# Kernel optimization log

Measured on AMD Instinct MI355X. Metric: run time of the kernel, lower is better.

The kernel has to match this reference:

```python
import jax, jax.numpy as jnp
import numpy as np
from jax import lax

EPS = 1e-8


def setup_inputs() -> dict:
    key = jax.random.key(0)
    k1, k2, k3, k4, k5 = jax.random.split(key, 5)
    b, c_in, c_out, h, w_sp, k, z = 8, 256, 256, 128, 128, 3, 512
    return {
        "x": jax.random.normal(k1, (b, c_in, h, w_sp), dtype=jnp.float32),
        "w": jax.random.normal(k2, (b, z), dtype=jnp.float32),
        "weight": jax.random.normal(k3, (c_out, c_in, k, k), dtype=jnp.float32),
        "affine_w": jax.random.normal(k4, (c_in, z), dtype=jnp.float32) * 0.02,
        "affine_b": jax.random.normal(k5, (c_in,), dtype=jnp.float32) * 0.02,
    }


def reference(x, w, weight, affine_w, affine_b):
    # style: [b, c_in] -> broadcast over (out_ch, kh, kw); +1 as in StyleGAN2
    style = w @ affine_w.T + affine_b + 1.0                      # [b, c_in]
    wgt = weight[None] * style[:, None, :, None, None]           # [b, O, I, kh, kw]
    # demodulation
    denom = lax.rsqrt(jnp.sum(wgt * wgt, axis=(2, 3, 4)) + EPS)  # [b, O]
    wgt = wgt * denom[:, :, None, None, None]

    # per-sample conv (equivalent to groups=b grouped conv), 'same' padding
    def conv_one(xi, wi):
        # xi: [I, H, W], wi: [O, I, kh, kw]
        return lax.conv_general_dilated(
            xi[None], wi, window_strides=(1, 1), padding="SAME",
            dimension_numbers=("NCHW", "OIHW", "NCHW"))[0]

    return jax.vmap(conv_one)(x, wgt)                            # [b, O, H, W]
```

## Files before the change

kernel.cpp:

```cpp
#include <hip/hip_runtime.h>

#define EPS 1e-8f

using short8 = __attribute__((ext_vector_type(8))) short;
using f32x16 = __attribute__((ext_vector_type(16))) float;
typedef unsigned short u16;

#define WAITV(N) asm volatile("s_waitcnt vmcnt(" #N ")" ::: "memory")
#define BARRIER() do { __builtin_amdgcn_s_barrier(); \
                       asm volatile("" ::: "memory"); } while (0)

__device__ __forceinline__ u16 f2bf(float f) {
    union { float f; unsigned u; } v; v.f = f;
    unsigned u = v.u;
    return (u16)((u + 0x7FFFu + ((u >> 16) & 1u)) >> 16);
}

__device__ __forceinline__ void g2l16(const void* gsrc, void* ldst) {
    __builtin_amdgcn_global_load_lds(
        (const __attribute__((address_space(1))) unsigned int*)gsrc,
        (__attribute__((address_space(3))) unsigned int*)ldst, 16, 0, 0);
}

__global__ void style_kernel(const float* __restrict__ w,
                             const float* __restrict__ affine_w,
                             const float* __restrict__ affine_b,
                             float* __restrict__ style) {
    int b = blockIdx.x;
    int i = threadIdx.x;
    __shared__ float wb[512];
    for (int z = threadIdx.x; z < 512; z += 256) wb[z] = w[b * 512 + z];
    __syncthreads();
    const float* aw = affine_w + i * 512;
    float acc = 0.f;
#pragma unroll 4
    for (int z = 0; z < 512; z += 4) {
        float4 a4 = *reinterpret_cast<const float4*>(aw + z);
        acc += a4.x * wb[z] + a4.y * wb[z + 1] + a4.z * wb[z + 2] + a4.w * wb[z + 3];
    }
    style[b * 256 + i] = acc + affine_b[i] + 1.0f;
}

__global__ void modw_kernel(const float* __restrict__ weight,
                            const float* __restrict__ style,
                            u16* __restrict__ wgt) {
    int b = blockIdx.x >> 8;
    int o = blockIdx.x & 255;
    int ic = threadIdx.x;
    float s = style[b * 256 + ic];
    const float* wp = weight + (size_t)(o * 256 + ic) * 9;
    float m[9];
    float ss = 0.f;
#pragma unroll
    for (int t = 0; t < 9; ++t) { m[t] = wp[t] * s; ss += m[t] * m[t]; }
#pragma unroll
    for (int off = 32; off > 0; off >>= 1) ss += __shfl_down(ss, off);
    __shared__ float part[4];
    int lane = threadIdx.x & 63, wid = threadIdx.x >> 6;
    if (lane == 0) part[wid] = ss;
    __syncthreads();
    float denom = rsqrtf(part[0] + part[1] + part[2] + part[3] + EPS);
    int g = ic >> 3, j = ic & 7;
#pragma unroll
    for (int t = 0; t < 9; ++t) {
        size_t idx = ((((size_t)(b * 9 + t) * 32 + g) * 256 + o) << 3) + j;
        wgt[idx] = f2bf(m[t] * denom);
    }
}

__global__ __launch_bounds__(256) void xform_kernel(const float* __restrict__ x,
                                                    u16* __restrict__ xb) {
    int s = blockIdx.x * 256 + threadIdx.x;
    int w = s & 127, h = (s >> 7) & 127, g = (s >> 14) & 31, b = s >> 19;
    const float* xp = x + (((size_t)(b * 256 + g * 8) * 128 + h) * 128 + w);
    union { u16 u[8]; short8 v; } pk;
#pragma unroll
    for (int j = 0; j < 8; ++j) pk.u[j] = f2bf(xp[(size_t)j * 16384]);
    *reinterpret_cast<short8*>(&xb[(size_t)s * 8]) = pk.v;
}

__global__ __launch_bounds__(256, 2) void conv_kernel(
    const u16* __restrict__ xb,
    const u16* __restrict__ wgt,
    float* __restrict__ out) {

    __shared__ __align__(16) u16 Xs[4][4][130][8];
    __shared__ __align__(16) u16 As[5][4][128][8];
    __shared__ __align__(16) u16 trash[1024];

    int bid = blockIdx.x;
    int swz = (bid & 7) * 128 + (bid >> 3);
    int ht = swz & 63, ot = (swz >> 6) & 1, b = swz >> 7;
    int h0 = ht * 2;

    int tid = threadIdx.x, lane = tid & 63, wid = tid >> 6;
    int wm = wid >> 1, wr = wid & 1;
    int l31 = lane & 31, lh = lane >> 5;

    auto stageA = [&](int cc, int tt, int ring) {
        const u16* wbase = wgt + ((size_t)(b * 9 + tt) * 32) * 2048;
#pragma unroll
        for (int k = 0; k < 2; ++k) {
            int seg = wid * 2 + k, g = seg >> 1, oh = seg & 1;
            const u16* src = wbase +
                ((size_t)(cc * 4 + g) * 256 + ot * 128 + oh * 64 + lane) * 8;
            g2l16(src, &As[ring][g][oh * 64][0]);
        }
    };

    {
        short8 z = {0, 0, 0, 0, 0, 0, 0, 0};
        short8* p0 = reinterpret_cast<short8*>(&Xs[0][0][0][0]);
        for (int i = tid; i < 2080; i += 256) p0[i] = z;
    }
    __syncthreads();

    stageA(0, 0, 0); stageA(0, 1, 1); stageA(0, 2, 2);
    {
        int hr = h0 + wid - 1;
        bool oob = ((unsigned)hr >= 128u);
        int hc = oob ? 0 : hr;
#pragma unroll
        for (int k = 0; k < 8; ++k) {
            int g = k >> 1, half = k & 1;
            const u16* src = xb +
                ((((size_t)(b * 32 + g)) * 128 + hc) * 128 + half * 64 + lane) * 8;
            void* dst = oob ? (void*)trash : (void*)&Xs[wid][g][1 + half * 64][0];
            g2l16(src, dst);
        }
    }
    WAITV(0);
    BARRIER();

    f32x16 acc[2][4] = {};
    short8 xr[8];
    int rr = 0, rw = 3, cs = 0, ts = 3;

    auto doPhase = [&](int t, int ring) {
        int kh = t / 3, kw = t - kh * 3;
        short8 af[2][2], bx8[2][4];
#pragma unroll
        for (int kk = 0; kk < 2; ++kk)
#pragma unroll
            for (int mi = 0; mi < 2; ++mi)
                af[kk][mi] = *reinterpret_cast<const short8*>(
                    &As[ring][kk * 2 + lh][wm * 64 + mi * 32 + l31][0]);
#pragma unroll
        for (int kk = 0; kk < 2; ++kk)
#pragma unroll
            for (int ni = 0; ni < 4; ++ni)
                bx8[kk][ni] = *reinterpret_cast<const short8*>(
                    &Xs[wr + kh][kk * 2 + lh][ni * 32 + l31 + kw][0]);
        __builtin_amdgcn_s_setprio(1);
#pragma unroll
        for (int mi = 0; mi < 2; ++mi)
#pragma unroll
            for (int ni = 0; ni < 4; ++ni)
#pragma unroll
                for (int kk = 0; kk < 2; ++kk)
                    acc[mi][ni] = __builtin_amdgcn_mfma_f32_32x32x16_bf16(
                        af[kk][mi], bx8[kk][ni], acc[mi][ni], 0, 0, 0);
        __builtin_amdgcn_s_setprio(0);
    };

    int hr = h0 + wid - 1;
    bool hValid = ((unsigned)hr < 128u);
    int hc = hValid ? hr : 0;

    for (int c = 0; c < 7; ++c) {
#pragma unroll
        for (int t = 0; t < 9; ++t) {
            stageA(cs, ts, rw);
            if (++ts == 9) { ts = 0; ++cs; }
            if (t == 5) {
#pragma unroll
                for (int k = 0; k < 8; ++k) {
                    int g = k >> 1, half = k & 1;
                    xr[k] = *reinterpret_cast<const short8*>(xb +
                        ((((size_t)(b * 32 + (c + 1) * 4 + g)) * 128 + hc) * 128 +
                         half * 64 + lane) * 8);
                }
            }
            doPhase(t, rr);
            rr = (rr == 4) ? 0 : rr + 1;
            rw = (rw == 4) ? 0 : rw + 1;
            if (t == 1 || t == 3) { WAITV(2);  BARRIER(); }
            else if (t == 5)      { WAITV(10); BARRIER(); }
            else if (t == 7)      { WAITV(12); BARRIER(); }
            else if (t == 8) {
                WAITV(2);
                BARRIER();
                if (hValid) {
#pragma unroll
                    for (int k = 0; k < 8; ++k) {
                        int g = k >> 1, half = k & 1;
                        *reinterpret_cast<short8*>(
                            &Xs[wid][g][1 + half * 64 + lane][0]) = xr[k];
                    }
                }
                asm volatile("s_waitcnt lgkmcnt(0)" ::: "memory");
                BARRIER();
            }
        }
    }
#pragma unroll
    for (int t = 0; t < 9; ++t) {
        if (t <= 5) {
            stageA(cs, ts, rw);
            if (++ts == 9) { ts = 0; ++cs; }
            rw = (rw == 4) ? 0 : rw + 1;
        }
        doPhase(t, rr);
        rr = (rr == 4) ? 0 : rr + 1;
        if (t == 1 || t == 3 || t == 5) { WAITV(2); BARRIER(); }
        else if (t == 7)                { WAITV(0); BARRIER(); }
    }

    int h = h0 + wr;
#pragma unroll
    for (int mi = 0; mi < 2; ++mi) {
        int ob = ot * 128 + wm * 64 + mi * 32 + 4 * lh;
#pragma unroll
        for (int ni = 0; ni < 4; ++ni) {
            int w_ = ni * 32 + l31;
#pragma unroll
            for (int reg = 0; reg < 16; ++reg) {
                int o = ob + (reg & 3) + 8 * (reg >> 2);
                out[(((size_t)(b * 256 + o) * 128 + h) * 128) + w_] = acc[mi][ni][reg];
            }
        }
    }
}

extern "C" void kernel_launch(void* const* d_in, const int* in_sizes, int n_in,
                              void* d_out, int out_size, void* d_ws, size_t ws_size,
                              hipStream_t stream) {
    const float* x        = (const float*)d_in[0];
    const float* w        = (const float*)d_in[1];
    const float* weight   = (const float*)d_in[2];
    const float* affine_w = (const float*)d_in[3];
    const float* affine_b = (const float*)d_in[4];
    float* out = (float*)d_out;

    float* style = (float*)d_ws;
    u16* wgt = (u16*)((char*)d_ws + 8192);
    u16* xbuf = (u16*)((char*)d_ws + 8192 + 9437184);

    xform_kernel<<<16384, 256, 0, stream>>>(x, xbuf);
    style_kernel<<<8, 256, 0, stream>>>(w, affine_w, affine_b, style);
    modw_kernel<<<2048, 256, 0, stream>>>(weight, style, wgt);
    conv_kernel<<<1024, 256, 0, stream>>>(xbuf, wgt, out);
}
```

Measured before the change: 209.1 us.

## Load weight fragments directly to registers and double-buffer X tiles in LDS

The weight (A) operand no longer passes through a 5-deep LDS ring. Each wave reads its MFMA fragments straight from global memory into registers, prefetching one tap ahead. The input rows are double-buffered in LDS with async global-to-LDS loads, so there is one barrier per channel chunk instead of several per chunk. This removes LDS traffic and barriers for A, at the cost of more global or L2 load latency exposed per tap. Waves sharing the same weights also load redundantly, and the vmcnt accounting now mixes register and LDS loads.

```diff
diff --git a/kernel.cpp b/kernel.cpp
--- a/kernel.cpp
+++ b/kernel.cpp
@@ -84,8 +84,7 @@
     const u16* __restrict__ wgt,
     float* __restrict__ out) {
 
-    __shared__ __align__(16) u16 Xs[4][4][130][8];
-    __shared__ __align__(16) u16 As[5][4][128][8];
+    __shared__ __align__(16) u16 Xs[2][4][4][130][8];
     __shared__ __align__(16) u16 trash[1024];
 
     int bid = blockIdx.x;
@@ -97,123 +96,81 @@
     int wm = wid >> 1, wr = wid & 1;
     int l31 = lane & 31, lh = lane >> 5;
 
-    auto stageA = [&](int cc, int tt, int ring) {
-        const u16* wbase = wgt + ((size_t)(b * 9 + tt) * 32) * 2048;
-#pragma unroll
-        for (int k = 0; k < 2; ++k) {
-            int seg = wid * 2 + k, g = seg >> 1, oh = seg & 1;
-            const u16* src = wbase +
-                ((size_t)(cc * 4 + g) * 256 + ot * 128 + oh * 64 + lane) * 8;
-            g2l16(src, &As[ring][g][oh * 64][0]);
-        }
+    int hr = h0 + wid - 1;
+    bool hValid = ((unsigned)hr < 128u);
+    int hc = hValid ? hr : 0;
+
+    const u16* aBase = wgt + ((size_t)(b * 9) * 32 * 256 +
+                              (size_t)(lh * 256 + ot * 128 + wm * 64 + l31)) * 8;
+
+    auto loadA = [&](short8 dst[2][2], int c, int t) {
+#pragma unroll
+        for (int kk = 0; kk < 2; ++kk)
+#pragma unroll
+            for (int mi = 0; mi < 2; ++mi)
+                dst[kk][mi] = *reinterpret_cast<const short8*>(
+                    aBase + (size_t)(((t * 32) + c * 4 + kk * 2) * 256 + mi * 32) * 8);
     };
-
-    {
-        short8 z = {0, 0, 0, 0, 0, 0, 0, 0};
-        short8* p0 = reinterpret_cast<short8*>(&Xs[0][0][0][0]);
-        for (int i = tid; i < 2080; i += 256) p0[i] = z;
-    }
-    __syncthreads();
-
-    stageA(0, 0, 0); stageA(0, 1, 1); stageA(0, 2, 2);
-    {
-        int hr = h0 + wid - 1;
-        bool oob = ((unsigned)hr >= 128u);
-        int hc = oob ? 0 : hr;
+    auto stageX = [&](int c1, int bx) {
 #pragma unroll
         for (int k = 0; k < 8; ++k) {
             int g = k >> 1, half = k & 1;
             const u16* src = xb +
-                ((((size_t)(b * 32 + g)) * 128 + hc) * 128 + half * 64 + lane) * 8;
-            void* dst = oob ? (void*)trash : (void*)&Xs[wid][g][1 + half * 64][0];
+                ((((size_t)(b * 32 + c1 * 4 + g)) * 128 + hc) * 128 + half * 64 + lane) * 8;
+            void* dst = hValid ? (void*)&Xs[bx][wid][g][1 + half * 64][0] : (void*)trash;
             g2l16(src, dst);
         }
-    }
-    WAITV(0);
+    };
+
+    {
+        short8 z = {0, 0, 0, 0, 0, 0, 0, 0};
+        short8* p0 = reinterpret_cast<short8*>(&Xs[0][0][0][0][0]);
+        for (int i = tid; i < 4160; i += 256) p0[i] = z;
+    }
+    __syncthreads();
+
+    short8 afC[2][2], afN[2][2];
+    stageX(0, 0);
+    loadA(afC, 0, 0);
+    WAITV(4);
     BARRIER();
 
     f32x16 acc[2][4] = {};
-    short8 xr[8];
-    int rr = 0, rw = 3, cs = 0, ts = 3;
-
-    auto doPhase = [&](int t, int ring) {
-        int kh = t / 3, kw = t - kh * 3;
-        short8 af[2][2], bx8[2][4];
-#pragma unroll
-        for (int kk = 0; kk < 2; ++kk)
+
+    for (int c = 0; c < 8; ++c) {
+        int buf = c & 1;
+#pragma unroll
+        for (int t = 0; t < 9; ++t) {
+            if (!(c == 7 && t == 8))
+                loadA(afN, t < 8 ? c : c + 1, t < 8 ? t + 1 : 0);
+            if (t == 0 && c < 7) stageX(c + 1, buf ^ 1);
+
+            int kh = t / 3, kw = t - kh * 3;
+            short8 bx8[2][4];
+#pragma unroll
+            for (int kk = 0; kk < 2; ++kk)
+#pragma unroll
+                for (int ni = 0; ni < 4; ++ni)
+                    bx8[kk][ni] = *reinterpret_cast<const short8*>(
+                        &Xs[buf][wr + kh][kk * 2 + lh][ni * 32 + l31 + kw][0]);
+            __builtin_amdgcn_s_setprio(1);
 #pragma unroll
             for (int mi = 0; mi < 2; ++mi)
-                af[kk][mi] = *reinterpret_cast<const short8*>(
-                    &As[ring][kk * 2 + lh][wm * 64 + mi * 32 + l31][0]);
-#pragma unroll
-        for (int kk = 0; kk < 2; ++kk)
-#pragma unroll
-            for (int ni = 0; ni < 4; ++ni)
-                bx8[kk][ni] = *reinterpret_cast<const short8*>(
-                    &Xs[wr + kh][kk * 2 + lh][ni * 32 + l31 + kw][0]);
-        __builtin_amdgcn_s_setprio(1);
-#pragma unroll
-        for (int mi = 0; mi < 2; ++mi)
-#pragma unroll
-            for (int ni = 0; ni < 4; ++ni)
-#pragma unroll
-                for (int kk = 0; kk < 2; ++kk)
-                    acc[mi][ni] = __builtin_amdgcn_mfma_f32_32x32x16_bf16(
-                        af[kk][mi], bx8[kk][ni], acc[mi][ni], 0, 0, 0);
-        __builtin_amdgcn_s_setprio(0);
-    };
-
-    int hr = h0 + wid - 1;
-    bool hValid = ((unsigned)hr < 128u);
-    int hc = hValid ? hr : 0;
-
-    for (int c = 0; c < 7; ++c) {
-#pragma unroll
-        for (int t = 0; t < 9; ++t) {
-            stageA(cs, ts, rw);
-            if (++ts == 9) { ts = 0; ++cs; }
-            if (t == 5) {
-#pragma unroll
-                for (int k = 0; k < 8; ++k) {
-                    int g = k >> 1, half = k & 1;
-                    xr[k] = *reinterpret_cast<const short8*>(xb +
-                        ((((size_t)(b * 32 + (c + 1) * 4 + g)) * 128 + hc) * 128 +
-                         half * 64 + lane) * 8);
-                }
-            }
-            doPhase(t, rr);
-            rr = (rr == 4) ? 0 : rr + 1;
-            rw = (rw == 4) ? 0 : rw + 1;
-            if (t == 1 || t == 3) { WAITV(2);  BARRIER(); }
-            else if (t == 5)      { WAITV(10); BARRIER(); }
-            else if (t == 7)      { WAITV(12); BARRIER(); }
-            else if (t == 8) {
-                WAITV(2);
-                BARRIER();
-                if (hValid) {
-#pragma unroll
-                    for (int k = 0; k < 8; ++k) {
-                        int g = k >> 1, half = k & 1;
-                        *reinterpret_cast<short8*>(
-                            &Xs[wid][g][1 + half * 64 + lane][0]) = xr[k];
-                    }
-                }
-                asm volatile("s_waitcnt lgkmcnt(0)" ::: "memory");
-                BARRIER();
-            }
+#pragma unroll
+                for (int ni = 0; ni < 4; ++ni)
+#pragma unroll
+                    for (int kk = 0; kk < 2; ++kk)
+                        acc[mi][ni] = __builtin_amdgcn_mfma_f32_32x32x16_bf16(
+                            afC[kk][mi], bx8[kk][ni], acc[mi][ni], 0, 0, 0);
+            __builtin_amdgcn_s_setprio(0);
+#pragma unroll
+            for (int kk = 0; kk < 2; ++kk)
+#pragma unroll
+                for (int mi = 0; mi < 2; ++mi)
+                    afC[kk][mi] = afN[kk][mi];
         }
-    }
-#pragma unroll
-    for (int t = 0; t < 9; ++t) {
-        if (t <= 5) {
-            stageA(cs, ts, rw);
-            if (++ts == 9) { ts = 0; ++cs; }
-            rw = (rw == 4) ? 0 : rw + 1;
-        }
-        doPhase(t, rr);
-        rr = (rr == 4) ? 0 : rr + 1;
-        if (t == 1 || t == 3 || t == 5) { WAITV(2); BARRIER(); }
-        else if (t == 7)                { WAITV(0); BARRIER(); }
+        WAITV(4);
+        BARRIER();
     }
 
     int h = h0 + wr;
```

New measurement: 196.3 us. 1.07x faster.
